# Kernel optimization log

Measured on AMD Instinct MI355X. Metric: run time of the kernel, lower is better.

Reference implementation:

```python
import jax, jax.numpy as jnp
import numpy as np

B, T, I = 8, 128, 196
TEXT_DIM, IMAGE_DIM, HIDDEN = 768, 1024, 512


def setup_inputs() -> dict:
    key = jax.random.key(0)
    ks = jax.random.split(key, 7)
    s = lambda d: 1.0 / np.sqrt(d)
    return {
        "text_features": jax.random.normal(ks[0], (B, T, TEXT_DIM), jnp.float32),
        "image_features": jax.random.normal(ks[1], (B, I, IMAGE_DIM), jnp.float32),
        "Wt": jax.random.normal(ks[2], (TEXT_DIM, HIDDEN), jnp.float32) * s(TEXT_DIM),
        "bt": jax.random.normal(ks[3], (HIDDEN,), jnp.float32) * s(TEXT_DIM),
        "Wi": jax.random.normal(ks[4], (IMAGE_DIM, HIDDEN), jnp.float32) * s(IMAGE_DIM),
        "bi": jax.random.normal(ks[5], (HIDDEN,), jnp.float32) * s(IMAGE_DIM),
        "wa": jax.random.normal(ks[6], (HIDDEN,), jnp.float32) * s(HIDDEN),
        "ba": jnp.zeros((1,), jnp.float32),
    }


def reference(text_features, image_features, Wt, bt, Wi, bi, wa, ba):
    # projections: [B,T,H] and [B,I,H]
    pt = jnp.einsum("btd,dh->bth", text_features, Wt) + bt
    pi = jnp.einsum("bid,dh->bih", image_features, Wi) + bi
    # additive Bahdanau scores: tanh of broadcast sum [B,T,I,H], reduced by wa
    h = jnp.tanh(pt[:, :, None, :] + pi[:, None, :, :])
    scores = jnp.einsum("btih,h->bti", h, wa) + ba[0]  # [B,T,I]
    text_attended = jnp.einsum("bti,bid->btd", jax.nn.softmax(scores, axis=-1), image_features)
    image_attended = jnp.einsum("bti,btd->bid", jax.nn.softmax(scores, axis=1), text_features)
    return text_attended, image_attended
```

## Files before the change

### kernel.cpp

```cpp
#include <hip/hip_runtime.h>
#include <math.h>

#define B 8
#define T 128
#define I_TOK 196
#define TEXT_DIM 768
#define IMAGE_DIM 1024
#define HIDDEN 512
#define EXP_SCALE 2.88539008177792681f

#if __has_builtin(__builtin_amdgcn_exp2f)
#define FAST_EXP2(x) __builtin_amdgcn_exp2f(x)
#else
#define FAST_EXP2(x) exp2f(x)
#endif
#if __has_builtin(__builtin_amdgcn_rcpf)
#define FAST_RCP(x) __builtin_amdgcn_rcpf(x)
#else
#define FAST_RCP(x) __fdividef(1.f, (x))
#endif

typedef short bf16x8 __attribute__((ext_vector_type(8)));
typedef float f32x4 __attribute__((ext_vector_type(4)));

typedef __attribute__((address_space(3))) void       as3_void;
typedef __attribute__((address_space(1))) const void as1_cvoid;

#define KT_T (TEXT_DIM / 32)
#define KT_I (IMAGE_DIM / 32)
#define MT_T (B * T / 16)
#define MT_I (B * I_TOK / 16)
#define NT   (HIDDEN / 16)

#define XT_ELEMS (MT_T * KT_T * 512)
#define XI_ELEMS (MT_I * KT_I * 512)
#define X_ELEMS  (XT_ELEMS + XI_ELEMS)
#define WT_T_ELEMS (NT * KT_T * 512)
#define W_ELEMS (WT_T_ELEMS + NT * KT_I * 512)

#define XTILES_T (MT_T * KT_T)
#define XTILES   (XTILES_T + MT_I * KT_I)
#define WTILES_T (NT * KT_T)
#define WTILES   (WTILES_T + NT * KT_I)
#define PREP_GRID ((XTILES + WTILES) / 4)

__device__ __forceinline__ unsigned short f2bf(float x) {
    unsigned int u = __float_as_uint(x);
    unsigned int r = u + 0x7FFFu + ((u >> 16) & 1u);
    return (unsigned short)(r >> 16);
}
__device__ __forceinline__ float bf2f(unsigned short h) {
    return __uint_as_float(((unsigned int)h) << 16);
}

__global__ __launch_bounds__(256) void prep_kernel(
        const float* __restrict__ text, const float* __restrict__ image,
        const float* __restrict__ Wt, const float* __restrict__ Wi,
        unsigned short* __restrict__ Xh, unsigned short* __restrict__ Xl,
        unsigned short* __restrict__ WTh, unsigned short* __restrict__ WTl)
{
    const int tid = threadIdx.x;
    const int lane = tid & 63, wv = tid >> 6;
    const int r16 = lane & 15, quad = lane >> 4;
    const int id = blockIdx.x * 4 + wv;

    float v[8];
    unsigned short* oh;
    unsigned short* ol;
    long dst;

    if (id < XTILES) {
        const float* X; int K, mt, kt;
        if (id < XTILES_T) { X = text; K = TEXT_DIM; mt = id / KT_T; kt = id % KT_T; }
        else { const int i2 = id - XTILES_T; X = image; K = IMAGE_DIM; mt = i2 / KT_I; kt = i2 % KT_I; }
        const float* src = X + (long)(mt * 16 + r16) * K + kt * 32 + quad * 8;
        const float4 a = *(const float4*)src;
        const float4 b = *(const float4*)(src + 4);
        v[0]=a.x; v[1]=a.y; v[2]=a.z; v[3]=a.w; v[4]=b.x; v[5]=b.y; v[6]=b.z; v[7]=b.w;
        oh = (id < XTILES_T) ? Xh : Xh + XT_ELEMS;
        ol = (id < XTILES_T) ? Xl : Xl + XT_ELEMS;
        const long tile = (id < XTILES_T) ? id : (long)(id - XTILES_T);
        dst = tile * 512 + lane * 8;
    } else {
        const int idw = id - XTILES;
        const float* W; int K, nt, kt;
        if (idw < WTILES_T) { W = Wt; K = TEXT_DIM; nt = idw / KT_T; kt = idw % KT_T; }
        else { const int i2 = idw - WTILES_T; W = Wi; K = IMAGE_DIM; nt = i2 / KT_I; kt = i2 % KT_I; }
        const float* src = W + (long)(kt * 32 + quad * 8) * HIDDEN + nt * 16 + r16;
        #pragma unroll
        for (int j = 0; j < 8; ++j) v[j] = src[(long)j * HIDDEN];
        oh = (idw < WTILES_T) ? WTh : WTh + WT_T_ELEMS;
        ol = (idw < WTILES_T) ? WTl : WTl + WT_T_ELEMS;
        const long tile = (idw < WTILES_T) ? idw : (long)(idw - WTILES_T);
        dst = tile * 512 + lane * 8;
    }

    uint4 hv, lv;
    unsigned int hh[8], ll[8];
    #pragma unroll
    for (int j = 0; j < 8; ++j) {
        hh[j] = f2bf(v[j]);
        ll[j] = f2bf(v[j] - bf2f((unsigned short)hh[j]));
    }
    hv.x = hh[0] | (hh[1] << 16); hv.y = hh[2] | (hh[3] << 16);
    hv.z = hh[4] | (hh[5] << 16); hv.w = hh[6] | (hh[7] << 16);
    lv.x = ll[0] | (ll[1] << 16); lv.y = ll[2] | (ll[3] << 16);
    lv.z = ll[4] | (ll[5] << 16); lv.w = ll[6] | (ll[7] << 16);
    *(uint4*)(oh + dst) = hv;
    *(uint4*)(ol + dst) = lv;
}

#define GT2_BLOCKS (16 * 8)
#define GI2_BLOCKS (25 * 8)
#define GEMM_GRID (GT2_BLOCKS + GI2_BLOCKS)

__global__ __launch_bounds__(256, 2) void mfma_proj_kernel(
        const unsigned short* __restrict__ Xh, const unsigned short* __restrict__ Xl,
        const unsigned short* __restrict__ WTh, const unsigned short* __restrict__ WTl,
        const float* __restrict__ bt, const float* __restrict__ bi,
        float* __restrict__ pt, float* __restrict__ pi)
{
    __shared__ __align__(16) unsigned short lds[2][16][512];

    const int tid = threadIdx.x;
    const int lane = tid & 63, wv = tid >> 6;
    const int r16 = lane & 15, quad = lane >> 4;
    const int wr = wv >> 1, wc = wv & 1;

    const int bid0 = blockIdx.x;
    int bid;
    if (bid0 < GT2_BLOCKS) bid = (bid0 & 7) * 16 + (bid0 >> 3);
    else { const int d = bid0 - GT2_BLOCKS; bid = GT2_BLOCKS + (d & 7) * 25 + (d >> 3); }

    const unsigned short *xh, *xl, *wh, *wl; const float* bias; float* Y;
    int ktiles, mt0;
    int n8;
    if (bid < GT2_BLOCKS) {
        xh = Xh; xl = Xl; wh = WTh; wl = WTl; bias = bt; Y = pt; ktiles = KT_T;
        mt0 = (bid >> 3) * 4; n8 = bid & 7;
    } else {
        const int ib = bid - GT2_BLOCKS;
        xh = Xh + XT_ELEMS; xl = Xl + XT_ELEMS;
        wh = WTh + WT_T_ELEMS; wl = WTl + WT_T_ELEMS;
        bias = bi; Y = pi; ktiles = KT_I;
        const int mg = ib >> 3;
        mt0 = (mg == 24) ? (MT_I - 4) : mg * 4;
        n8 = ib & 7;
    }
    const int nt0 = n8 * 4;

    const unsigned short* ssrc[4];
    #pragma unroll
    for (int q = 0; q < 4; ++q) {
        const int t = wv * 4 + q;
        const int g = t >> 2;
        const int i = t & 3;
        const unsigned short* base = (g == 0) ? xh : (g == 1) ? xl : (g == 2) ? wh : wl;
        const long row = (g < 2) ? (long)(mt0 + i) : (long)(nt0 + i);
        ssrc[q] = base + row * ktiles * 512 + lane * 8;
    }

#define STAGE(buf, kt) do {                                                    \
        _Pragma("unroll")                                                      \
        for (int q_ = 0; q_ < 4; ++q_) {                                       \
            __builtin_amdgcn_global_load_lds(                                  \
                (as1_cvoid*)(ssrc[q_] + (long)(kt) * 512),                     \
                (as3_void*)&lds[buf][wv * 4 + q_][0], 16, 0, 0);               \
        } } while (0)

    f32x4 a00 = {0,0,0,0}, a01 = {0,0,0,0}, a10 = {0,0,0,0}, a11 = {0,0,0,0};

    STAGE(0, 0);
    __syncthreads();

    int cur = 0;
    for (int s = 0; s < ktiles; ++s) {
        if (s + 1 < ktiles) STAGE(cur ^ 1, s + 1);

        const int fo = lane * 8;
        const bf16x8 Ah0 = *(const bf16x8*)&lds[cur][wr * 2 + 0][fo];
        const bf16x8 Ah1 = *(const bf16x8*)&lds[cur][wr * 2 + 1][fo];
        const bf16x8 Al0 = *(const bf16x8*)&lds[cur][4 + wr * 2 + 0][fo];
        const bf16x8 Al1 = *(const bf16x8*)&lds[cur][4 + wr * 2 + 1][fo];
        const bf16x8 Bh0 = *(const bf16x8*)&lds[cur][8 + wc * 2 + 0][fo];
        const bf16x8 Bh1 = *(const bf16x8*)&lds[cur][8 + wc * 2 + 1][fo];
        const bf16x8 Bl0 = *(const bf16x8*)&lds[cur][12 + wc * 2 + 0][fo];
        const bf16x8 Bl1 = *(const bf16x8*)&lds[cur][12 + wc * 2 + 1][fo];

        a00 = __builtin_amdgcn_mfma_f32_16x16x32_bf16(Ah0, Bh0, a00, 0, 0, 0);
        a01 = __builtin_amdgcn_mfma_f32_16x16x32_bf16(Ah0, Bh1, a01, 0, 0, 0);
        a10 = __builtin_amdgcn_mfma_f32_16x16x32_bf16(Ah1, Bh0, a10, 0, 0, 0);
        a11 = __builtin_amdgcn_mfma_f32_16x16x32_bf16(Ah1, Bh1, a11, 0, 0, 0);
        a00 = __builtin_amdgcn_mfma_f32_16x16x32_bf16(Ah0, Bl0, a00, 0, 0, 0);
        a01 = __builtin_amdgcn_mfma_f32_16x16x32_bf16(Ah0, Bl1, a01, 0, 0, 0);
        a10 = __builtin_amdgcn_mfma_f32_16x16x32_bf16(Ah1, Bl0, a10, 0, 0, 0);
        a11 = __builtin_amdgcn_mfma_f32_16x16x32_bf16(Ah1, Bl1, a11, 0, 0, 0);
        a00 = __builtin_amdgcn_mfma_f32_16x16x32_bf16(Al0, Bh0, a00, 0, 0, 0);
        a01 = __builtin_amdgcn_mfma_f32_16x16x32_bf16(Al0, Bh1, a01, 0, 0, 0);
        a10 = __builtin_amdgcn_mfma_f32_16x16x32_bf16(Al1, Bh0, a10, 0, 0, 0);
        a11 = __builtin_amdgcn_mfma_f32_16x16x32_bf16(Al1, Bh1, a11, 0, 0, 0);

        __syncthreads();
        cur ^= 1;
    }
#undef STAGE

    const int row00 = (mt0 + wr * 2) * 16 + quad * 4;
    const int col0  = (nt0 + wc * 2) * 16 + r16;
    const float bv0 = bias[col0];
    const float bv1 = bias[col0 + 16];
    #pragma unroll
    for (int r = 0; r < 4; ++r) {
        Y[(long)(row00 + r)      * HIDDEN + col0]      = FAST_EXP2((a00[r] + bv0) * EXP_SCALE);
        Y[(long)(row00 + r)      * HIDDEN + col0 + 16] = FAST_EXP2((a01[r] + bv1) * EXP_SCALE);
        Y[(long)(row00 + 16 + r) * HIDDEN + col0]      = FAST_EXP2((a10[r] + bv0) * EXP_SCALE);
        Y[(long)(row00 + 16 + r) * HIDDEN + col0 + 16] = FAST_EXP2((a11[r] + bv1) * EXP_SCALE);
    }
}

__global__ __launch_bounds__(256, 4) void scores_kernel(const float* __restrict__ pt,
        const float* __restrict__ pi, const float* __restrict__ wa,
        const float* __restrict__ ba, float* __restrict__ scores)
{
    const int blk = blockIdx.x;
    const int half = blk & 1;
    const int bt0 = (blk >> 1) * 2;
    const int b = bt0 >> 7;
    const int tid = threadIdx.x;
    const int lane = tid & 63, wave = tid >> 6;

    const float* ptrow = pt + (long)bt0 * HIDDEN + lane * 8;
    const float4 pA0 = *(const float4*)ptrow;
    const float4 pB0 = *(const float4*)(ptrow + 4);
    const float4 pA1 = *(const float4*)(ptrow + HIDDEN);
    const float4 pB1 = *(const float4*)(ptrow + HIDDEN + 4);
    float4 wA = *(const float4*)(wa + lane * 8);
    float4 wB = *(const float4*)(wa + lane * 8 + 4);

    float S = wA.x + wA.y + wA.z + wA.w + wB.x + wB.y + wB.z + wB.w;
    #pragma unroll
    for (int off = 32; off; off >>= 1) S += __shfl_down(S, off);
    const float base = S + ba[0];

    wA.x *= -2.f; wA.y *= -2.f; wA.z *= -2.f; wA.w *= -2.f;
    wB.x *= -2.f; wB.y *= -2.f; wB.z *= -2.f; wB.w *= -2.f;

    const float* pib = pi + (long)b * I_TOK * HIDDEN + lane * 8;
    const int i0 = half * 98 + wave;
    const int iend = half * 98 + 98;

    float4 ca = *(const float4*)(pib + (long)i0 * HIDDEN);
    float4 cb = *(const float4*)(pib + (long)i0 * HIDDEN + 4);

    for (int i = i0; i < iend; i += 4) {
        const int inx = (i + 4 < iend) ? (i + 4) : i;
        const float4 na = *(const float4*)(pib + (long)inx * HIDDEN);
        const float4 nb = *(const float4*)(pib + (long)inx * HIDDEN + 4);

        float acc0 = 0.f;
        acc0 = fmaf(wA.x, FAST_RCP(fmaf(pA0.x, ca.x, 1.f)), acc0);
        acc0 = fmaf(wA.y, FAST_RCP(fmaf(pA0.y, ca.y, 1.f)), acc0);
        acc0 = fmaf(wA.z, FAST_RCP(fmaf(pA0.z, ca.z, 1.f)), acc0);
        acc0 = fmaf(wA.w, FAST_RCP(fmaf(pA0.w, ca.w, 1.f)), acc0);
        acc0 = fmaf(wB.x, FAST_RCP(fmaf(pB0.x, cb.x, 1.f)), acc0);
        acc0 = fmaf(wB.y, FAST_RCP(fmaf(pB0.y, cb.y, 1.f)), acc0);
        acc0 = fmaf(wB.z, FAST_RCP(fmaf(pB0.z, cb.z, 1.f)), acc0);
        acc0 = fmaf(wB.w, FAST_RCP(fmaf(pB0.w, cb.w, 1.f)), acc0);

        float acc1 = 0.f;
        acc1 = fmaf(wA.x, FAST_RCP(fmaf(pA1.x, ca.x, 1.f)), acc1);
        acc1 = fmaf(wA.y, FAST_RCP(fmaf(pA1.y, ca.y, 1.f)), acc1);
        acc1 = fmaf(wA.z, FAST_RCP(fmaf(pA1.z, ca.z, 1.f)), acc1);
        acc1 = fmaf(wA.w, FAST_RCP(fmaf(pA1.w, ca.w, 1.f)), acc1);
        acc1 = fmaf(wB.x, FAST_RCP(fmaf(pB1.x, cb.x, 1.f)), acc1);
        acc1 = fmaf(wB.y, FAST_RCP(fmaf(pB1.y, cb.y, 1.f)), acc1);
        acc1 = fmaf(wB.z, FAST_RCP(fmaf(pB1.z, cb.z, 1.f)), acc1);
        acc1 = fmaf(wB.w, FAST_RCP(fmaf(pB1.w, cb.w, 1.f)), acc1);

        #pragma unroll
        for (int off = 32; off; off >>= 1) {
            acc0 += __shfl_down(acc0, off);
            acc1 += __shfl_down(acc1, off);
        }
        if (lane == 0) {
            scores[(long)bt0 * I_TOK + i]       = base + acc0;
            scores[(long)(bt0 + 1) * I_TOK + i] = base + acc1;
        }
        ca = na; cb = nb;
    }
}

#define ATT_P1_BLOCKS 256
#define ATT_P2_BLOCKS (B * 28)
#define ATT_GRID (ATT_P1_BLOCKS + ATT_P2_BLOCKS)

__global__ __launch_bounds__(256) void att_kernel(const float* __restrict__ scores,
        const float* __restrict__ image, const float* __restrict__ text,
        float* __restrict__ out_text, float* __restrict__ out_img)
{
    const int tid = threadIdx.x, lane = tid & 63, wave = tid >> 6;

    if (blockIdx.x < ATT_P1_BLOCKS) {
        const int bid = blockIdx.x;
        const int csplit = bid & 1;
        const int grp = bid >> 1;
        const int b = grp >> 4;
        const int t0 = (grp & 15) * 8;

        __shared__ float ps[I_TOK][8];
        #pragma unroll
        for (int rr = 0; rr < 2; ++rr) {
            const int tsub = wave + rr * 4;
            const float* srow = scores + ((long)(b * T + t0 + tsub)) * I_TOK;
            const float s0 = srow[lane];
            const float s1 = srow[lane + 64];
            const float s2 = srow[lane + 128];
            const float s3 = (lane < 4) ? srow[lane + 192] : -INFINITY;
            float m = fmaxf(fmaxf(s0, s1), fmaxf(s2, s3));
            #pragma unroll
            for (int off = 32; off; off >>= 1) m = fmaxf(m, __shfl_xor(m, off));
            const float e0 = __expf(s0 - m);
            const float e1 = __expf(s1 - m);
            const float e2 = __expf(s2 - m);
            const float e3 = (lane < 4) ? __expf(s3 - m) : 0.f;
            float sum = e0 + e1 + e2 + e3;
            #pragma unroll
            for (int off = 32; off; off >>= 1) sum += __shfl_xor(sum, off);
            const float inv = __fdividef(1.0f, sum);
            ps[lane][tsub] = e0 * inv;
            ps[lane + 64][tsub] = e1 * inv;
            ps[lane + 128][tsub] = e2 * inv;
            if (lane < 4) ps[lane + 192][tsub] = e3 * inv;
        }
        __syncthreads();

        const float* img = image + (long)b * I_TOK * IMAGE_DIM + csplit * 512 + tid * 2;
        float2 a0 = {0,0}, a1 = {0,0}, a2 = {0,0}, a3 = {0,0};
        float2 a4 = {0,0}, a5 = {0,0}, a6 = {0,0}, a7 = {0,0};

        float2 v0 = *(const float2*)(img + 0 * IMAGE_DIM);
        float2 v1 = *(const float2*)(img + 1 * IMAGE_DIM);
        float2 v2 = *(const float2*)(img + 2 * IMAGE_DIM);
        float2 v3 = *(const float2*)(img + 3 * IMAGE_DIM);
        float4 pL0 = *(const float4*)&ps[0][0]; float4 pH0 = *(const float4*)&ps[0][4];
        float4 pL1 = *(const float4*)&ps[1][0]; float4 pH1 = *(const float4*)&ps[1][4];
        float4 pL2 = *(const float4*)&ps[2][0]; float4 pH2 = *(const float4*)&ps[2][4];
        float4 pL3 = *(const float4*)&ps[3][0]; float4 pH3 = *(const float4*)&ps[3][4];

        for (int g = 0; g < 49; ++g) {
            const int ib = (g + 1 < 49) ? (g + 1) * 4 : g * 4;
            const float2 w0 = *(const float2*)(img + (long)(ib + 0) * IMAGE_DIM);
            const float2 w1 = *(const float2*)(img + (long)(ib + 1) * IMAGE_DIM);
            const float2 w2 = *(const float2*)(img + (long)(ib + 2) * IMAGE_DIM);
            const float2 w3 = *(const float2*)(img + (long)(ib + 3) * IMAGE_DIM);
            const float4 nL0 = *(const float4*)&ps[ib + 0][0]; const float4 nH0 = *(const float4*)&ps[ib + 0][4];
            const float4 nL1 = *(const float4*)&ps[ib + 1][0]; const float4 nH1 = *(const float4*)&ps[ib + 1][4];
            const float4 nL2 = *(const float4*)&ps[ib + 2][0]; const float4 nH2 = *(const float4*)&ps[ib + 2][4];
            const float4 nL3 = *(const float4*)&ps[ib + 3][0]; const float4 nH3 = *(const float4*)&ps[ib + 3][4];

#define ATT_ROW(vr, pl, ph)                                                   \
            a0.x = fmaf(pl.x, vr.x, a0.x); a0.y = fmaf(pl.x, vr.y, a0.y);     \
            a1.x = fmaf(pl.y, vr.x, a1.x); a1.y = fmaf(pl.y, vr.y, a1.y);     \
            a2.x = fmaf(pl.z, vr.x, a2.x); a2.y = fmaf(pl.z, vr.y, a2.y);     \
            a3.x = fmaf(pl.w, vr.x, a3.x); a3.y = fmaf(pl.w, vr.y, a3.y);     \
            a4.x = fmaf(ph.x, vr.x, a4.x); a4.y = fmaf(ph.x, vr.y, a4.y);     \
            a5.x = fmaf(ph.y, vr.x, a5.x); a5.y = fmaf(ph.y, vr.y, a5.y);     \
            a6.x = fmaf(ph.z, vr.x, a6.x); a6.y = fmaf(ph.z, vr.y, a6.y);     \
            a7.x = fmaf(ph.w, vr.x, a7.x); a7.y = fmaf(ph.w, vr.y, a7.y);
            ATT_ROW(v0, pL0, pH0)
            ATT_ROW(v1, pL1, pH1)
            ATT_ROW(v2, pL2, pH2)
            ATT_ROW(v3, pL3, pH3)
#undef ATT_ROW
            v0 = w0; v1 = w1; v2 = w2; v3 = w3;
            pL0 = nL0; pH0 = nH0; pL1 = nL1; pH1 = nH1;
            pL2 = nL2; pH2 = nH2; pL3 = nL3; pH3 = nH3;
        }
        float* o = out_text + ((long)(b * T + t0)) * IMAGE_DIM + csplit * 512 + tid * 2;
        *(float2*)(o + 0 * IMAGE_DIM) = a0;
        *(float2*)(o + 1 * IMAGE_DIM) = a1;
        *(float2*)(o + 2 * IMAGE_DIM) = a2;
        *(float2*)(o + 3 * IMAGE_DIM) = a3;
        *(float2*)(o + 4 * IMAGE_DIM) = a4;
        *(float2*)(o + 5 * IMAGE_DIM) = a5;
        *(float2*)(o + 6 * IMAGE_DIM) = a6;
        *(float2*)(o + 7 * IMAGE_DIM) = a7;
    } else {
        const int bid = blockIdx.x - ATT_P1_BLOCKS;
        const int b = bid / 28;
        const int i0 = (bid % 28) * 7;

        __shared__ float qs[T][8];
        for (int cc = wave; cc < 7; cc += 4) {
            const float* sc = scores + (long)b * T * I_TOK + (i0 + cc);
            const float s0 = sc[(long)lane * I_TOK];
            const float s1 = sc[(long)(lane + 64) * I_TOK];
            float m = fmaxf(s0, s1);
            #pragma unroll
            for (int off = 32; off; off >>= 1) m = fmaxf(m, __shfl_xor(m, off));
            const float e0 = __expf(s0 - m);
            const float e1 = __expf(s1 - m);
            float sum = e0 + e1;
            #pragma unroll
            for (int off = 32; off; off >>= 1) sum += __shfl_xor(sum, off);
            const float inv = __fdividef(1.0f, sum);
            qs[lane][cc] = e0 * inv;
            qs[lane + 64][cc] = e1 * inv;
        }
        __syncthreads();

        const float* txt2 = text + (long)b * T * TEXT_DIM + tid * 2;
        const float* txt1 = text + (long)b * T * TEXT_DIM + 512 + tid;
        float ax[7], ay[7], az[7];
        #pragma unroll
        for (int r = 0; r < 7; ++r) { ax[r] = 0.f; ay[r] = 0.f; az[r] = 0.f; }

        float2 u0 = *(const float2*)(txt2 + 0 * TEXT_DIM);
        float2 u1 = *(const float2*)(txt2 + 1 * TEXT_DIM);
        float  z0 = txt1[0 * TEXT_DIM];
        float  z1 = txt1[1 * TEXT_DIM];
        float4 qa0 = *(const float4*)&qs[0][0]; float4 qb0 = *(const float4*)&qs[0][4];
        float4 qa1 = *(const float4*)&qs[1][0]; float4 qb1 = *(const float4*)&qs[1][4];

        for (int g = 0; g < 64; ++g) {
            const int tb = (g + 1 < 64) ? (g + 1) * 2 : g * 2;
            const float2 nu0 = *(const float2*)(txt2 + (long)(tb + 0) * TEXT_DIM);
            const float2 nu1 = *(const float2*)(txt2 + (long)(tb + 1) * TEXT_DIM);
            const float  nz0 = txt1[(long)(tb + 0) * TEXT_DIM];
            const float  nz1 = txt1[(long)(tb + 1) * TEXT_DIM];
            const float4 na0 = *(const float4*)&qs[tb + 0][0];
            const float4 nb0 = *(const float4*)&qs[tb + 0][4];
            const float4 na1 = *(const float4*)&qs[tb + 1][0];
            const float4 nb1 = *(const float4*)&qs[tb + 1][4];

            ax[0] = fmaf(qa0.x, u0.x, ax[0]); ay[0] = fmaf(qa0.x, u0.y, ay[0]); az[0] = fmaf(qa0.x, z0, az[0]);
            ax[1] = fmaf(qa0.y, u0.x, ax[1]); ay[1] = fmaf(qa0.y, u0.y, ay[1]); az[1] = fmaf(qa0.y, z0, az[1]);
            ax[2] = fmaf(qa0.z, u0.x, ax[2]); ay[2] = fmaf(qa0.z, u0.y, ay[2]); az[2] = fmaf(qa0.z, z0, az[2]);
            ax[3] = fmaf(qa0.w, u0.x, ax[3]); ay[3] = fmaf(qa0.w, u0.y, ay[3]); az[3] = fmaf(qa0.w, z0, az[3]);
            ax[4] = fmaf(qb0.x, u0.x, ax[4]); ay[4] = fmaf(qb0.x, u0.y, ay[4]); az[4] = fmaf(qb0.x, z0, az[4]);
            ax[5] = fmaf(qb0.y, u0.x, ax[5]); ay[5] = fmaf(qb0.y, u0.y, ay[5]); az[5] = fmaf(qb0.y, z0, az[5]);
            ax[6] = fmaf(qb0.z, u0.x, ax[6]); ay[6] = fmaf(qb0.z, u0.y, ay[6]); az[6] = fmaf(qb0.z, z0, az[6]);
            ax[0] = fmaf(qa1.x, u1.x, ax[0]); ay[0] = fmaf(qa1.x, u1.y, ay[0]); az[0] = fmaf(qa1.x, z1, az[0]);
            ax[1] = fmaf(qa1.y, u1.x, ax[1]); ay[1] = fmaf(qa1.y, u1.y, ay[1]); az[1] = fmaf(qa1.y, z1, az[1]);
            ax[2] = fmaf(qa1.z, u1.x, ax[2]); ay[2] = fmaf(qa1.z, u1.y, ay[2]); az[2] = fmaf(qa1.z, z1, az[2]);
            ax[3] = fmaf(qa1.w, u1.x, ax[3]); ay[3] = fmaf(qa1.w, u1.y, ay[3]); az[3] = fmaf(qa1.w, z1, az[3]);
            ax[4] = fmaf(qb1.x, u1.x, ax[4]); ay[4] = fmaf(qb1.x, u1.y, ay[4]); az[4] = fmaf(qb1.x, z1, az[4]);
            ax[5] = fmaf(qb1.y, u1.x, ax[5]); ay[5] = fmaf(qb1.y, u1.y, ay[5]); az[5] = fmaf(qb1.y, z1, az[5]);
            ax[6] = fmaf(qb1.z, u1.x, ax[6]); ay[6] = fmaf(qb1.z, u1.y, ay[6]); az[6] = fmaf(qb1.z, z1, az[6]);

            u0 = nu0; u1 = nu1; z0 = nz0; z1 = nz1;
            qa0 = na0; qb0 = nb0; qa1 = na1; qb1 = nb1;
        }
        float* o = out_img + ((long)b * I_TOK + i0) * TEXT_DIM;
        #pragma unroll
        for (int r = 0; r < 7; ++r) {
            float2 w;
            w.x = ax[r]; w.y = ay[r];
            *(float2*)(o + (long)r * TEXT_DIM + tid * 2) = w;
            o[(long)r * TEXT_DIM + 512 + tid] = az[r];
        }
    }
}

extern "C" void kernel_launch(void* const* d_in, const int* in_sizes, int n_in,
                              void* d_out, int out_size, void* d_ws, size_t ws_size,
                              hipStream_t stream) {
    const float* text  = (const float*)d_in[0];
    const float* image = (const float*)d_in[1];
    const float* Wt    = (const float*)d_in[2];
    const float* bt    = (const float*)d_in[3];
    const float* Wi    = (const float*)d_in[4];
    const float* bi    = (const float*)d_in[5];
    const float* wa    = (const float*)d_in[6];
    const float* ba    = (const float*)d_in[7];

    float* pt = (float*)d_ws;
    float* pi = pt + (long)B * T * HIDDEN;
    float* sc = pi + (long)B * I_TOK * HIDDEN;
    unsigned short* Xh  = (unsigned short*)(sc + (long)B * T * I_TOK);
    unsigned short* Xl  = Xh + X_ELEMS;
    unsigned short* WTh = Xl + X_ELEMS;
    unsigned short* WTl = WTh + W_ELEMS;

    float* out_text = (float*)d_out;
    float* out_img  = out_text + (long)B * T * IMAGE_DIM;

    prep_kernel<<<PREP_GRID, 256, 0, stream>>>(text, image, Wt, Wi, Xh, Xl, WTh, WTl);
    mfma_proj_kernel<<<GEMM_GRID, 256, 0, stream>>>(Xh, Xl, WTh, WTl, bt, bi, pt, pi);
    scores_kernel<<<B * T, 256, 0, stream>>>(pt, pi, wa, ba, sc);
    att_kernel<<<ATT_GRID, 256, 0, stream>>>(sc, image, text, out_text, out_img);
}
```

Measured before the change: 142.4 us.

## Fuse four kernels into one persistent kernel with software grid barriers

The prep, projection GEMM, scores and attention kernels are merged into a single 512-block persistent kernel. The stages are separated by atomic-counter grid barriers, and the counters are zeroed with a memset before launch. This is meant to remove the launch gaps and tail idle time between the four dependent kernel launches. In exchange it relies on all 512 blocks being co-resident, otherwise the barriers deadlock. It also forces one shared-memory and register budget across all stages, and stages that use fewer blocks leave the rest idle at the barrier.

```diff
diff --git a/kernel.cpp b/kernel.cpp
--- a/kernel.cpp
+++ b/kernel.cpp
@@ -42,7 +42,17 @@
 #define XTILES   (XTILES_T + MT_I * KT_I)
 #define WTILES_T (NT * KT_T)
 #define WTILES   (WTILES_T + NT * KT_I)
-#define PREP_GRID ((XTILES + WTILES) / 4)
+#define ALL_TILES (XTILES + WTILES)
+
+#define GT2_BLOCKS (16 * 8)
+#define GI2_BLOCKS (25 * 8)
+#define GEMM_GRID (GT2_BLOCKS + GI2_BLOCKS)
+
+#define ATT_P1_BLOCKS 256
+#define ATT_P2_BLOCKS (B * 28)
+#define ATT_GRID (ATT_P1_BLOCKS + ATT_P2_BLOCKS)
+
+#define MEGA_GRID 512
 
 __device__ __forceinline__ unsigned short f2bf(float x) {
     unsigned int u = __float_as_uint(x);
@@ -53,16 +63,27 @@
     return __uint_as_float(((unsigned int)h) << 16);
 }
 
-__global__ __launch_bounds__(256) void prep_kernel(
+__device__ __forceinline__ void grid_barrier(unsigned int* bar, int ph) {
+    __syncthreads();
+    if (threadIdx.x == 0) {
+        __threadfence();
+        atomicAdd(&bar[ph], 1u);
+        while (__hip_atomic_load(&bar[ph], __ATOMIC_RELAXED, __HIP_MEMORY_SCOPE_AGENT)
+               < (unsigned int)MEGA_GRID)
+            __builtin_amdgcn_s_sleep(2);
+    }
+    __syncthreads();
+    __threadfence();
+}
+
+__device__ __forceinline__ void prep_tile(const int id,
         const float* __restrict__ text, const float* __restrict__ image,
         const float* __restrict__ Wt, const float* __restrict__ Wi,
         unsigned short* __restrict__ Xh, unsigned short* __restrict__ Xl,
         unsigned short* __restrict__ WTh, unsigned short* __restrict__ WTl)
 {
-    const int tid = threadIdx.x;
-    const int lane = tid & 63, wv = tid >> 6;
+    const int lane = threadIdx.x & 63;
     const int r16 = lane & 15, quad = lane >> 4;
-    const int id = blockIdx.x * 4 + wv;
 
     float v[8];
     unsigned short* oh;
@@ -110,31 +131,24 @@
     *(uint4*)(ol + dst) = lv;
 }
 
-#define GT2_BLOCKS (16 * 8)
-#define GI2_BLOCKS (25 * 8)
-#define GEMM_GRID (GT2_BLOCKS + GI2_BLOCKS)
-
-__global__ __launch_bounds__(256, 2) void mfma_proj_kernel(
+__device__ __forceinline__ void proj_block(const int bid0,
+        unsigned short (*lds)[16][512],
         const unsigned short* __restrict__ Xh, const unsigned short* __restrict__ Xl,
         const unsigned short* __restrict__ WTh, const unsigned short* __restrict__ WTl,
         const float* __restrict__ bt, const float* __restrict__ bi,
         float* __restrict__ pt, float* __restrict__ pi)
 {
-    __shared__ __align__(16) unsigned short lds[2][16][512];
-
     const int tid = threadIdx.x;
     const int lane = tid & 63, wv = tid >> 6;
     const int r16 = lane & 15, quad = lane >> 4;
     const int wr = wv >> 1, wc = wv & 1;
 
-    const int bid0 = blockIdx.x;
     int bid;
     if (bid0 < GT2_BLOCKS) bid = (bid0 & 7) * 16 + (bid0 >> 3);
     else { const int d = bid0 - GT2_BLOCKS; bid = GT2_BLOCKS + (d & 7) * 25 + (d >> 3); }
 
     const unsigned short *xh, *xl, *wh, *wl; const float* bias; float* Y;
-    int ktiles, mt0;
-    int n8;
+    int ktiles, mt0, n8;
     if (bid < GT2_BLOCKS) {
         xh = Xh; xl = Xl; wh = WTh; wl = WTl; bias = bt; Y = pt; ktiles = KT_T;
         mt0 = (bid >> 3) * 4; n8 = bid & 7;
@@ -218,11 +232,11 @@
     }
 }
 
-__global__ __launch_bounds__(256, 4) void scores_kernel(const float* __restrict__ pt,
-        const float* __restrict__ pi, const float* __restrict__ wa,
-        const float* __restrict__ ba, float* __restrict__ scores)
+__device__ __forceinline__ void scores_block(const int blk,
+        const float* __restrict__ pt, const float* __restrict__ pi,
+        const float* __restrict__ wa, const float* __restrict__ ba,
+        float* __restrict__ scores)
 {
-    const int blk = blockIdx.x;
     const int half = blk & 1;
     const int bt0 = (blk >> 1) * 2;
     const int b = bt0 >> 7;
@@ -290,24 +304,21 @@
     }
 }
 
-#define ATT_P1_BLOCKS 256
-#define ATT_P2_BLOCKS (B * 28)
-#define ATT_GRID (ATT_P1_BLOCKS + ATT_P2_BLOCKS)
-
-__global__ __launch_bounds__(256) void att_kernel(const float* __restrict__ scores,
+__device__ __forceinline__ void att_block(const int bid0, unsigned char* smem,
+        const float* __restrict__ scores,
         const float* __restrict__ image, const float* __restrict__ text,
         float* __restrict__ out_text, float* __restrict__ out_img)
 {
     const int tid = threadIdx.x, lane = tid & 63, wave = tid >> 6;
 
-    if (blockIdx.x < ATT_P1_BLOCKS) {
-        const int bid = blockIdx.x;
+    if (bid0 < ATT_P1_BLOCKS) {
+        const int bid = bid0;
         const int csplit = bid & 1;
         const int grp = bid >> 1;
         const int b = grp >> 4;
         const int t0 = (grp & 15) * 8;
 
-        __shared__ float ps[I_TOK][8];
+        float (*ps)[8] = (float (*)[8])smem;
         #pragma unroll
         for (int rr = 0; rr < 2; ++rr) {
             const int tsub = wave + rr * 4;
@@ -386,11 +397,11 @@
         *(float2*)(o + 6 * IMAGE_DIM) = a6;
         *(float2*)(o + 7 * IMAGE_DIM) = a7;
     } else {
-        const int bid = blockIdx.x - ATT_P1_BLOCKS;
+        const int bid = bid0 - ATT_P1_BLOCKS;
         const int b = bid / 28;
         const int i0 = (bid % 28) * 7;
 
-        __shared__ float qs[T][8];
+        float (*qs)[8] = (float (*)[8])smem;
         for (int cc = wave; cc < 7; cc += 4) {
             const float* sc = scores + (long)b * T * I_TOK + (i0 + cc);
             const float s0 = sc[(long)lane * I_TOK];
@@ -462,6 +473,39 @@
     }
 }
 
+__global__ __launch_bounds__(256, 2) void mega_kernel(
+        const float* __restrict__ text, const float* __restrict__ image,
+        const float* __restrict__ Wt, const float* __restrict__ bt,
+        const float* __restrict__ Wi, const float* __restrict__ bi,
+        const float* __restrict__ wa, const float* __restrict__ ba,
+        unsigned short* __restrict__ Xh, unsigned short* __restrict__ Xl,
+        unsigned short* __restrict__ WTh, unsigned short* __restrict__ WTl,
+        float* __restrict__ pt, float* __restrict__ pi, float* __restrict__ sc,
+        float* __restrict__ out_text, float* __restrict__ out_img,
+        unsigned int* __restrict__ bar)
+{
+    __shared__ __align__(16) unsigned char smem[32768];
+    const int wv = threadIdx.x >> 6;
+
+    for (int base = 0; base < ALL_TILES; base += MEGA_GRID * 4) {
+        const int id = base + blockIdx.x * 4 + wv;
+        if (id < ALL_TILES) prep_tile(id, text, image, Wt, Wi, Xh, Xl, WTh, WTl);
+    }
+    grid_barrier(bar, 0);
+
+    if (blockIdx.x < GEMM_GRID)
+        proj_block(blockIdx.x, (unsigned short (*)[16][512])smem,
+                   Xh, Xl, WTh, WTl, bt, bi, pt, pi);
+    grid_barrier(bar, 1);
+
+    scores_block(blockIdx.x * 2 + 0, pt, pi, wa, ba, sc);
+    scores_block(blockIdx.x * 2 + 1, pt, pi, wa, ba, sc);
+    grid_barrier(bar, 2);
+
+    if (blockIdx.x < ATT_GRID)
+        att_block(blockIdx.x, smem, sc, image, text, out_text, out_img);
+}
+
 extern "C" void kernel_launch(void* const* d_in, const int* in_sizes, int n_in,
                               void* d_out, int out_size, void* d_ws, size_t ws_size,
                               hipStream_t stream) {
@@ -481,12 +525,13 @@
     unsigned short* Xl  = Xh + X_ELEMS;
     unsigned short* WTh = Xl + X_ELEMS;
     unsigned short* WTl = WTh + W_ELEMS;
+    unsigned int*   bar = (unsigned int*)(WTl + W_ELEMS);
 
     float* out_text = (float*)d_out;
     float* out_img  = out_text + (long)B * T * IMAGE_DIM;
 
-    prep_kernel<<<PREP_GRID, 256, 0, stream>>>(text, image, Wt, Wi, Xh, Xl, WTh, WTl);
-    mfma_proj_kernel<<<GEMM_GRID, 256, 0, stream>>>(Xh, Xl, WTh, WTl, bt, bi, pt, pi);
-    scores_kernel<<<B * T, 256, 0, stream>>>(pt, pi, wa, ba, sc);
-    att_kernel<<<ATT_GRID, 256, 0, stream>>>(sc, image, text, out_text, out_img);
-}
+    hipMemsetAsync(bar, 0, 64, stream);
+    mega_kernel<<<MEGA_GRID, 256, 0, stream>>>(
+        text, image, Wt, bt, Wi, bi, wa, ba,
+        Xh, Xl, WTh, WTl, pt, pi, sc, out_text, out_img, bar);
+}
```

New measurement: 361.3 us. 2.54x slower.
